# Performance work log

Hardware: AMD Instinct MI355X
Metric: run time of the kernel (lower is better)

## Reference

```python
import jax, jax.numpy as jnp
import numpy as np

H_DIM = 2048
N_HEADS = 16

def setup_inputs() -> dict:
    key = jax.random.key(0)
    ks = jax.random.split(key, 9)
    B, T, C = 2, 2048, H_DIM
    scale = 1.0 / np.sqrt(C)  # lecun_normal approx
    src = jax.random.normal(ks[0], (B, T, C), dtype=jnp.float32)
    Wq = jax.random.normal(ks[1], (C, H_DIM), dtype=jnp.float32) * scale
    Wk = jax.random.normal(ks[2], (C, H_DIM), dtype=jnp.float32) * scale
    Wv = jax.random.normal(ks[3], (C, H_DIM), dtype=jnp.float32) * scale
    Wo = jax.random.normal(ks[4], (H_DIM, H_DIM), dtype=jnp.float32) * scale
    bq = jnp.zeros((H_DIM,), jnp.float32)
    bk = jnp.zeros((H_DIM,), jnp.float32)
    bv = jnp.zeros((H_DIM,), jnp.float32)
    bo = jnp.zeros((H_DIM,), jnp.float32)
    return {"src": src, "Wq": Wq, "bq": bq, "Wk": Wk, "bk": bk,
            "Wv": Wv, "bv": bv, "Wo": Wo, "bo": bo}

def reference(src, Wq, bq, Wk, bk, Wv, bv, Wo, bo):
    B, T, C = src.shape
    N = N_HEADS
    D = C // N
    def heads(x):  # [B,T,h_dim] -> [B,N,T,D]
        return x.reshape(B, T, N, D).transpose(0, 2, 1, 3)
    q = heads(src @ Wq + bq)
    k = heads(src @ Wk + bk)
    v = heads(src @ Wv + bv)
    # scaled dot-product with causal mask
    scores = jnp.einsum('bntd,bnsd->bnts', q, k) / jnp.sqrt(jnp.float32(D))
    causal = jnp.tril(jnp.ones((T, T), dtype=bool))
    scores = jnp.where(causal[None, None], scores, -jnp.inf)
    attn = jax.nn.softmax(scores, axis=-1)
    out = jnp.einsum('bnts,bnsd->bntd', attn, v)  # dropout is identity (drop_p=0)
    out = out.transpose(0, 2, 1, 3).reshape(B, T, N * D)
    return out @ Wo + bo
```

## Files before the change

kernel.cpp:

```cpp
#include <hip/hip_runtime.h>
#include <hip/hip_bf16.h>

typedef float f32x4 __attribute__((ext_vector_type(4)));
typedef __bf16 bf16x8v __attribute__((ext_vector_type(8)));
typedef __bf16 bf16x4v __attribute__((ext_vector_type(4)));
typedef unsigned uint2v __attribute__((ext_vector_type(2)));
typedef bf16x8v __attribute__((may_alias)) bf16x8;
typedef bf16x4v __attribute__((may_alias)) bf16x4;
typedef uint2v __attribute__((may_alias)) u32x2;

typedef __attribute__((address_space(1))) const void gvoid_t;
typedef __attribute__((address_space(3))) void lvoid_t;

#define DEVINL __device__ __forceinline__

#define BDIM 2
#define TDIM 2048
#define CDIM 2048
#define NHEAD 16
#define DHEAD 128
#define MROWS 4096
#define WSZ ((size_t)CDIM * CDIM)
#define XSZ ((size_t)MROWS * CDIM)

#define BARRIER_LGKM() asm volatile("s_waitcnt lgkmcnt(0)\ns_barrier" ::: "memory")

DEVINL __bf16 f2bf(float f) {
  unsigned u = __builtin_bit_cast(unsigned, f);
  u += 0x7fffu + ((u >> 16) & 1u);
  unsigned short h = (unsigned short)(u >> 16);
  return __builtin_bit_cast(__bf16, h);
}

DEVINL unsigned pk2bf_trunc(float lo, float hi) {
  return __builtin_amdgcn_perm(__builtin_bit_cast(unsigned, hi),
                               __builtin_bit_cast(unsigned, lo), 0x07060302);
}

DEVINL void gl2lds16(const void* g, void* l) {
  __builtin_amdgcn_global_load_lds((gvoid_t*)g, (lvoid_t*)l, 16, 0, 0);
}

__global__ void detect_dtype(const unsigned* __restrict__ w,
                             int* __restrict__ flag, int* __restrict__ cnt) {
  const int l = threadIdx.x;
  if (l == 0) *cnt = 0;
  const unsigned word = w[l];
  const unsigned e = (word >> 7) & 0xFFu;
  const int vote = (e >= 0x70u && e <= 0x87u) ? 1 : 0;
  const unsigned long long m = __ballot(vote);
  if (l == 0) *flag = (__popcll(m) >= 32) ? 1 : 0;
}

__global__ __launch_bounds__(256) void cvt_src(const void* __restrict__ in,
                                               __bf16* __restrict__ out,
                                               const int* __restrict__ flag,
                                               int n8) {
  const int i = blockIdx.x * 256 + threadIdx.x;
  if (i >= n8) return;
  if (*flag) {
    ((bf16x8*)out)[i] = ((const bf16x8*)in)[i];
  } else {
    const float* f = (const float*)in + (size_t)i * 8;
    bf16x8v v;
#pragma unroll
    for (int j = 0; j < 8; ++j) v[j] = f2bf(f[j]);
    ((bf16x8*)out)[i] = v;
  }
}

__global__ __launch_bounds__(256) void cvt_wt(
    const void* __restrict__ w0, const void* __restrict__ w1,
    const void* __restrict__ w2, const void* __restrict__ w3,
    __bf16* __restrict__ out, const int* __restrict__ flag) {
  __shared__ __attribute__((aligned(16))) __bf16 tile[64][68];
  const void* W = (blockIdx.z == 0) ? w0 : (blockIdx.z == 1) ? w1
                : (blockIdx.z == 2) ? w2 : w3;
  __bf16* Wt = out + (size_t)blockIdx.z * WSZ;
  const int tx = threadIdx.x & 63, ty = threadIdx.x >> 6;
  const int k0 = blockIdx.x * 64, n0 = blockIdx.y * 64;
  const int fl = *flag;
#pragma unroll
  for (int i = ty; i < 64; i += 4) {
    const size_t off = (size_t)(k0 + i) * CDIM + n0 + tx;
    const float v = fl ? (float)((const __bf16*)W)[off] : ((const float*)W)[off];
    tile[i][tx] = f2bf(v);
  }
  __syncthreads();
#pragma unroll
  for (int i = ty; i < 64; i += 4)
    Wt[(size_t)(n0 + i) * CDIM + k0 + tx] = tile[tx][i];
}

__global__ __launch_bounds__(256) void cvt_bias(
    const void* __restrict__ b0, const void* __restrict__ b1,
    const void* __restrict__ b2, const void* __restrict__ b3,
    float* __restrict__ out, const int* __restrict__ flag) {
  const int i = blockIdx.x * 256 + threadIdx.x;
  const void* b = (i < 2048) ? b0 : (i < 4096) ? b1 : (i < 6144) ? b2 : b3;
  const int idx = i & 2047;
  out[i] = (*flag) ? (float)((const __bf16*)b)[idx] : ((const float*)b)[idx];
}

template <int MODE>
__global__ __launch_bounds__(512, 2) void gemmring(
    const __bf16* __restrict__ A, const __bf16* __restrict__ Bt,
    const float* __restrict__ bias, __bf16* __restrict__ qb,
    __bf16* __restrict__ kb, __bf16* __restrict__ vtb,
    const int* __restrict__ flag, void* __restrict__ outp) {
  constexpr int K = CDIM;
  constexpr int NKT = K / 64;
  __shared__ __attribute__((aligned(16))) __bf16 Asl[4][128 * 32];
  __shared__ __attribute__((aligned(16))) __bf16 Bsl[4][256 * 32];

  const int tid = threadIdx.x;
  const int w = tid >> 6, l = tid & 63;
  const int quad = l >> 4, l16 = l & 15;
  const int wm = w >> 2, wn = w & 3;

  const int bid = blockIdx.x;
  const int bm = bid & 31, bn = bid >> 5;
  const int m0 = bm * 128, n0 = bn * 256;

  const int ls = (tid & 7) ^ ((tid >> 3) & 7);
  const int rbase = 2 * (tid >> 3) + (ls >> 2);
  const int cb8 = (ls & 3) * 8;
  const __bf16* gAh = A + (size_t)(m0 + rbase) * K + cb8;
  const __bf16* gBh = Bt + (size_t)(n0 + rbase) * K + cb8;

  const int L2 = l16 >> 1;
  const int physr = (((l16 & 1) << 2) + quad) ^ L2;
  const int lane_e = L2 * 64 + physr * 8;

#define STAGE_A(h)                                                       \
  gl2lds16(gAh + (size_t)(((h) >> 1) * 64 + ((h) & 1) * 32),             \
           (__bf16*)Asl[(h) & 3] + w * 512)
#define STAGE_B(h, e)                                                    \
  gl2lds16(gBh + (size_t)(e) * 128 * K +                                 \
               (((h) >> 1) * 64 + ((h) & 1) * 32),                       \
           (__bf16*)Bsl[(h) & 3] + (e) * 4096 + w * 512)

  f32x4 acc[4][4];
#pragma unroll
  for (int i = 0; i < 4; ++i)
#pragma unroll
    for (int j = 0; j < 4; ++j) acc[i][j] = (f32x4){0.f, 0.f, 0.f, 0.f};

  STAGE_A(0); STAGE_B(0, 0); STAGE_B(0, 1);
  STAGE_A(1); STAGE_B(1, 0); STAGE_B(1, 1);
  STAGE_A(2); STAGE_B(2, 0); STAGE_B(2, 1);
  asm volatile("s_waitcnt vmcnt(6)" ::: "memory");
  __builtin_amdgcn_sched_barrier(0);
  __builtin_amdgcn_s_barrier();

#define MFMA8(NF0)                                                        \
  __builtin_amdgcn_s_setprio(1);                                          \
  _Pragma("unroll") for (int mi = 0; mi < 4; ++mi) {                      \
    acc[mi][(NF0)] = __builtin_amdgcn_mfma_f32_16x16x32_bf16(             \
        afr[mi], bfr[0], acc[mi][(NF0)], 0, 0, 0);                        \
    acc[mi][(NF0) + 1] = __builtin_amdgcn_mfma_f32_16x16x32_bf16(         \
        afr[mi], bfr[1], acc[mi][(NF0) + 1], 0, 0, 0);                    \
  }                                                                       \
  __builtin_amdgcn_s_setprio(0);

#define LGKM_BAR()                                                        \
  __builtin_amdgcn_s_barrier();                                           \
  asm volatile("s_waitcnt lgkmcnt(0)" ::: "memory");                      \
  __builtin_amdgcn_sched_barrier(0)

  for (int kt = 0; kt < NKT; ++kt) {
    const int h0 = 2 * kt;
    const __bf16* Ab0 = Asl[h0 & 3];
    const __bf16* Bb0 = Bsl[h0 & 3];
    const __bf16* Ab1 = Asl[(h0 + 1) & 3];
    const __bf16* Bb1 = Bsl[(h0 + 1) & 3];
    bf16x8 afr[4], bfr[2];

#pragma unroll
    for (int mi = 0; mi < 4; ++mi)
      afr[mi] = *(const bf16x8*)&Ab0[(wm * 64 + mi * 16) * 32 + lane_e];
    bfr[0] = *(const bf16x8*)&Bb0[(wn * 64 + 0 * 16) * 32 + lane_e];
    bfr[1] = *(const bf16x8*)&Bb0[(wn * 64 + 1 * 16) * 32 + lane_e];
    if (kt <= NKT - 2) { STAGE_A(h0 + 3); STAGE_B(h0 + 3, 0); }
    LGKM_BAR();
    MFMA8(0)
    __builtin_amdgcn_s_barrier();

    bfr[0] = *(const bf16x8*)&Bb0[(wn * 64 + 2 * 16) * 32 + lane_e];
    bfr[1] = *(const bf16x8*)&Bb0[(wn * 64 + 3 * 16) * 32 + lane_e];
    if (kt <= NKT - 2) { STAGE_B(h0 + 3, 1); }
    LGKM_BAR();
    MFMA8(2)
    if (kt < NKT - 1)
      asm volatile("s_waitcnt vmcnt(6)" ::: "memory");
    else
      asm volatile("s_waitcnt vmcnt(0)" ::: "memory");
    __builtin_amdgcn_sched_barrier(0);
    __builtin_amdgcn_s_barrier();

#pragma unroll
    for (int mi = 0; mi < 4; ++mi)
      afr[mi] = *(const bf16x8*)&Ab1[(wm * 64 + mi * 16) * 32 + lane_e];
    bfr[0] = *(const bf16x8*)&Bb1[(wn * 64 + 0 * 16) * 32 + lane_e];
    bfr[1] = *(const bf16x8*)&Bb1[(wn * 64 + 1 * 16) * 32 + lane_e];
    if (kt <= NKT - 3) { STAGE_A(h0 + 4); STAGE_B(h0 + 4, 0); }
    LGKM_BAR();
    MFMA8(0)
    __builtin_amdgcn_s_barrier();

    bfr[0] = *(const bf16x8*)&Bb1[(wn * 64 + 2 * 16) * 32 + lane_e];
    bfr[1] = *(const bf16x8*)&Bb1[(wn * 64 + 3 * 16) * 32 + lane_e];
    if (kt <= NKT - 3) { STAGE_B(h0 + 4, 1); }
    LGKM_BAR();
    MFMA8(2)
    if (kt < NKT - 2)
      asm volatile("s_waitcnt vmcnt(6)" ::: "memory");
    else if (kt == NKT - 2)
      asm volatile("s_waitcnt vmcnt(3)" ::: "memory");
    __builtin_amdgcn_sched_barrier(0);
    __builtin_amdgcn_s_barrier();
  }
#undef MFMA8
#undef LGKM_BAR
#undef STAGE_A
#undef STAGE_B

  if (MODE == 0) {
    const int mat = n0 >> 11;
#pragma unroll
    for (int nf = 0; nf < 4; ++nf) {
      const int n = n0 + wn * 64 + nf * 16 + l16;
      const int nn = n & 2047;
      const int h = nn >> 7, d = nn & 127;
      const float bv = bias[n];
#pragma unroll
      for (int mi = 0; mi < 4; ++mi) {
        const int mbase = m0 + wm * 64 + mi * 16 + quad * 4;
        const int bb = mbase >> 11, t = mbase & 2047;
        if (mat == 2) {
          bf16x4v v4;
#pragma unroll
          for (int r = 0; r < 4; ++r) v4[r] = f2bf(acc[mi][nf][r] + bv);
          *(bf16x4*)&vtb[((size_t)(bb * NHEAD + h) * DHEAD + d) * TDIM + t] = v4;
        } else {
          __bf16* op = (mat == 0) ? qb : kb;
#pragma unroll
          for (int r = 0; r < 4; ++r)
            op[((size_t)(bb * NHEAD + h) * TDIM + t + r) * DHEAD + d] =
                f2bf(acc[mi][nf][r] + bv);
        }
      }
    }
  } else {
    const int ofl = *flag;
#pragma unroll
    for (int nf = 0; nf < 4; ++nf) {
      const int n = n0 + wn * 64 + nf * 16 + l16;
      const float bv = bias[n];
#pragma unroll
      for (int mi = 0; mi < 4; ++mi) {
#pragma unroll
        for (int r = 0; r < 4; ++r) {
          const int m = m0 + wm * 64 + mi * 16 + quad * 4 + r;
          const float v = acc[mi][nf][r] + bv;
          if (ofl) ((__bf16*)outp)[(size_t)m * CDIM + n] = f2bf(v);
          else     ((float*)outp)[(size_t)m * CDIM + n] = v;
        }
      }
    }
  }
}

__global__ __launch_bounds__(256, 2) void attn(
    const __bf16* __restrict__ Q, const __bf16* __restrict__ K,
    const __bf16* __restrict__ Vt, __bf16* __restrict__ ctx,
    int* __restrict__ cnt) {
  constexpr float CSC = 0.12753139726f;
  __shared__ __attribute__((aligned(16))) __bf16 Kls[64 * 128];
  __shared__ __attribute__((aligned(16))) __bf16 Vls[128 * 64];
  __shared__ __attribute__((aligned(16))) __bf16 Pls[4][32 * 64];
  __shared__ int jobLds;

  const int tid = threadIdx.x;
  const int w = tid >> 6, l = tid & 63, quad = l >> 4, l16 = l & 15;

  const int krow = tid >> 4;
  const int kcol = tid & 15;
  const int kldsoff = ((kcol ^ krow) * 8);
  const int vrow = tid >> 3;
  const int vcol = tid & 7;
  const int vldsoff = ((vcol ^ (vrow & 7)) * 8);

  for (;;) {
    __syncthreads();
    if (tid == 0) jobLds = atomicAdd(cnt, 1);
    __syncthreads();
    const int j = jobLds;
    if (j >= 512) break;
    const int qt = 15 - (j >> 5);
    const int bh = j & 31;
    const int t0w = qt * 128 + w * 32;
    const __bf16* Qbh = Q + (size_t)bh * TDIM * DHEAD;
    const __bf16* Kbh = K + (size_t)bh * TDIM * DHEAD;
    const __bf16* Vbh = Vt + (size_t)bh * TDIM * DHEAD;

    bf16x8 qf[2][4];
#pragma unroll
    for (int tt = 0; tt < 2; ++tt)
#pragma unroll
      for (int ks = 0; ks < 4; ++ks)
        qf[tt][ks] = *(const bf16x8*)(Qbh +
                     (size_t)(t0w + tt * 16 + l16) * DHEAD + ks * 32 + quad * 8);

    f32x4 oacc[8][2];
#pragma unroll
    for (int dt = 0; dt < 8; ++dt)
#pragma unroll
      for (int tt = 0; tt < 2; ++tt) oacc[dt][tt] = (f32x4){0.f, 0.f, 0.f, 0.f};
    float mrow[2] = {-1e30f, -1e30f};
    float lrow[2] = {0.f, 0.f};

    const int nsb = 2 * (qt + 1);

    bf16x8 kr[4], vr[4];
#pragma unroll
    for (int p = 0; p < 4; ++p)
      kr[p] = *(const bf16x8*)(Kbh + (size_t)(p * 16 + krow) * DHEAD + kcol * 8);
#pragma unroll
    for (int p = 0; p < 4; ++p)
      vr[p] = *(const bf16x8*)(Vbh + (size_t)(p * 32 + vrow) * TDIM + vcol * 8);

    for (int sb = 0; sb < nsb; ++sb) {
      const int s0 = sb * 64;
      BARRIER_LGKM();
#pragma unroll
      for (int p = 0; p < 4; ++p)
        *(bf16x8*)&Kls[(p * 16 + krow) * 128 + kldsoff] = kr[p];
#pragma unroll
      for (int p = 0; p < 4; ++p)
        *(bf16x8*)&Vls[(p * 32 + vrow) * 64 + vldsoff] = vr[p];
      if (sb + 1 < nsb) {
        const int s1 = s0 + 64;
#pragma unroll
        for (int p = 0; p < 4; ++p)
          kr[p] = *(const bf16x8*)(Kbh + (size_t)(s1 + p * 16 + krow) * DHEAD +
                                   kcol * 8);
#pragma unroll
        for (int p = 0; p < 4; ++p)
          vr[p] = *(const bf16x8*)(Vbh + (size_t)(p * 32 + vrow) * TDIM + s1 +
                                   vcol * 8);
      }
      BARRIER_LGKM();
      if (s0 > t0w + 31) continue;

      f32x4 sacc[4][2];
#pragma unroll
      for (int st = 0; st < 4; ++st)
#pragma unroll
        for (int tt = 0; tt < 2; ++tt) sacc[st][tt] = (f32x4){0.f, 0.f, 0.f, 0.f};
#pragma unroll
      for (int ks = 0; ks < 4; ++ks) {
        bf16x8 kf[4];
#pragma unroll
        for (int st = 0; st < 4; ++st)
          kf[st] = *(const bf16x8*)&Kls[(st * 16 + l16) * 128 +
                                        (((ks * 4 + quad) ^ l16) * 8)];
#pragma unroll
        for (int st = 0; st < 4; ++st)
#pragma unroll
          for (int tt = 0; tt < 2; ++tt)
            sacc[st][tt] = __builtin_amdgcn_mfma_f32_16x16x32_bf16(
                kf[st], qf[tt][ks], sacc[st][tt], 0, 0, 0);
      }
      if (s0 + 63 > t0w) {
#pragma unroll
        for (int st = 0; st < 4; ++st)
#pragma unroll
          for (int tt = 0; tt < 2; ++tt)
#pragma unroll
            for (int r = 0; r < 4; ++r) {
              const int s = s0 + st * 16 + quad * 4 + r;
              const int t = t0w + tt * 16 + l16;
              if (s > t) sacc[st][tt][r] = -1e30f;
            }
      }
#pragma unroll
      for (int tt = 0; tt < 2; ++tt) {
        float vm = -1e30f;
#pragma unroll
        for (int st = 0; st < 4; ++st)
#pragma unroll
          for (int r = 0; r < 4; ++r) vm = fmaxf(vm, sacc[st][tt][r]);
        vm = fmaxf(vm, __shfl_xor(vm, 16));
        vm = fmaxf(vm, __shfl_xor(vm, 32));
        const float mnew = fmaxf(mrow[tt], vm);
        if (__ballot(mnew > mrow[tt])) {
          const float alpha = exp2f((mrow[tt] - mnew) * CSC);
          lrow[tt] *= alpha;
#pragma unroll
          for (int dt = 0; dt < 8; ++dt)
#pragma unroll
            for (int r = 0; r < 4; ++r) oacc[dt][tt][r] *= alpha;
          mrow[tt] = mnew;
        }
        float rs = 0.f;
#pragma unroll
        for (int st = 0; st < 4; ++st) {
          const float p0 = exp2f((sacc[st][tt][0] - mnew) * CSC);
          const float p1 = exp2f((sacc[st][tt][1] - mnew) * CSC);
          const float p2 = exp2f((sacc[st][tt][2] - mnew) * CSC);
          const float p3 = exp2f((sacc[st][tt][3] - mnew) * CSC);
          rs += (p0 + p1) + (p2 + p3);
          u32x2 pk = {pk2bf_trunc(p0, p1), pk2bf_trunc(p2, p3)};
          *(u32x2*)&Pls[w][(tt * 16 + l16) * 64 +
                           (((st * 2 + (quad >> 1)) ^ (l16 & 7)) * 8) +
                           (quad & 1) * 4] = pk;
        }
        rs += __shfl_xor(rs, 16);
        rs += __shfl_xor(rs, 32);
        lrow[tt] += rs;
      }
      asm volatile("s_waitcnt lgkmcnt(0)" ::: "memory");
#pragma unroll
      for (int ks = 0; ks < 2; ++ks) {
        bf16x8 pf[2];
#pragma unroll
        for (int tt = 0; tt < 2; ++tt)
          pf[tt] = *(const bf16x8*)&Pls[w][(tt * 16 + l16) * 64 +
                                           (((ks * 4 + quad) ^ (l16 & 7)) * 8)];
#pragma unroll
        for (int dt = 0; dt < 8; ++dt) {
          const bf16x8 vf =
              *(const bf16x8*)&Vls[(dt * 16 + l16) * 64 +
                                   (((ks * 4 + quad) ^ (l16 & 7)) * 8)];
#pragma unroll
          for (int tt = 0; tt < 2; ++tt)
            oacc[dt][tt] = __builtin_amdgcn_mfma_f32_16x16x32_bf16(
                vf, pf[tt], oacc[dt][tt], 0, 0, 0);
        }
      }
    }

    const int b = bh >> 4, h = bh & 15;
#pragma unroll
    for (int tt = 0; tt < 2; ++tt) {
      const float rinv = 1.0f / lrow[tt];
      const int t = t0w + tt * 16 + l16;
      __bf16* cp = ctx + ((size_t)(b * TDIM + t)) * CDIM + h * DHEAD;
#pragma unroll
      for (int dt = 0; dt < 8; ++dt) {
        bf16x4v v4;
#pragma unroll
        for (int r = 0; r < 4; ++r) v4[r] = f2bf(oacc[dt][tt][r] * rinv);
        *(bf16x4*)&cp[dt * 16 + quad * 4] = v4;
      }
    }
  }
}

extern "C" void kernel_launch(void* const* d_in, const int* in_sizes, int n_in,
                              void* d_out, int out_size, void* d_ws,
                              size_t ws_size, hipStream_t stream) {
  const void* src = d_in[0];
  const void* Wq = d_in[1];
  const void* bq = d_in[2];
  const void* Wk = d_in[3];
  const void* bk = d_in[4];
  const void* Wv = d_in[5];
  const void* bv = d_in[6];
  const void* Wo = d_in[7];
  const void* bo = d_in[8];

  char* wsb = (char*)d_ws;
  int* flag = (int*)wsb;
  int* cnt = (int*)(wsb + 128);
  __bf16* srcbf = (__bf16*)(wsb + 256);
  __bf16* wqt = srcbf + XSZ;
  __bf16* wkt = wqt + WSZ;
  __bf16* wvt = wkt + WSZ;
  __bf16* wot = wvt + WSZ;
  __bf16* qb = wot + WSZ;
  __bf16* kb = qb + XSZ;
  __bf16* vtb = kb + XSZ;
  float* biasf = (float*)(vtb + XSZ);
  __bf16* ctx = srcbf;

  detect_dtype<<<1, 64, 0, stream>>>((const unsigned*)src, flag, cnt);
  cvt_src<<<4096, 256, 0, stream>>>(src, srcbf, flag, (int)(XSZ / 8));
  cvt_wt<<<dim3(32, 32, 4), 256, 0, stream>>>(Wq, Wk, Wv, Wo, wqt, flag);
  cvt_bias<<<32, 256, 0, stream>>>(bq, bk, bv, bo, biasf, flag);
  gemmring<0><<<768, 512, 0, stream>>>(srcbf, wqt, biasf, qb, kb, vtb,
                                       nullptr, nullptr);
  attn<<<512, 256, 0, stream>>>(qb, kb, vtb, ctx, cnt);
  gemmring<1><<<256, 512, 0, stream>>>(ctx, wot, biasf + 6144, nullptr,
                                       nullptr, nullptr, flag, d_out);
}
```

Measured before the change: 426.6 us.

## Inline dtype detection, fuse bias conversion, lazy softmax rescale, MFMA priority

Removes the separate dtype-detect and bias-conversion launches by running a per-wave detection inside each kernel and folding bias conversion into extra blocks of the source-conversion kernel, with a memset for the counter. In attention, the running-max rescale is skipped unless the new max exceeds the old by a threshold, which cuts rescale work but lets exponentials run against a stale max. s_setprio is raised around the MFMA loops to favour matrix issue. Each wave now re-reads the source words to detect dtype, which adds small redundant loads.

```diff
diff --git a/kernel.cpp b/kernel.cpp
--- a/kernel.cpp
+++ b/kernel.cpp
@@ -41,24 +41,32 @@
   __builtin_amdgcn_global_load_lds((gvoid_t*)g, (lvoid_t*)l, 16, 0, 0);
 }
 
-__global__ void detect_dtype(const unsigned* __restrict__ w,
-                             int* __restrict__ flag, int* __restrict__ cnt) {
-  const int l = threadIdx.x;
-  if (l == 0) *cnt = 0;
+DEVINL int wave_detect(const unsigned* __restrict__ w) {
+  const int l = threadIdx.x & 63;
   const unsigned word = w[l];
   const unsigned e = (word >> 7) & 0xFFu;
   const int vote = (e >= 0x70u && e <= 0x87u) ? 1 : 0;
   const unsigned long long m = __ballot(vote);
-  if (l == 0) *flag = (__popcll(m) >= 32) ? 1 : 0;
-}
-
-__global__ __launch_bounds__(256) void cvt_src(const void* __restrict__ in,
-                                               __bf16* __restrict__ out,
-                                               const int* __restrict__ flag,
-                                               int n8) {
-  const int i = blockIdx.x * 256 + threadIdx.x;
+  return (__popcll(m) >= 32) ? 1 : 0;
+}
+
+__global__ __launch_bounds__(256) void cvt_src(
+    const void* __restrict__ in, __bf16* __restrict__ out, int n8,
+    const void* __restrict__ b0, const void* __restrict__ b1,
+    const void* __restrict__ b2, const void* __restrict__ b3,
+    float* __restrict__ biasf) {
+  const int fl = wave_detect((const unsigned*)in);
+  const int bi = blockIdx.x;
+  if (bi >= 4096) {
+    const int i = (bi - 4096) * 256 + threadIdx.x;
+    const void* b = (i < 2048) ? b0 : (i < 4096) ? b1 : (i < 6144) ? b2 : b3;
+    const int idx = i & 2047;
+    biasf[i] = fl ? (float)((const __bf16*)b)[idx] : ((const float*)b)[idx];
+    return;
+  }
+  const int i = bi * 256 + threadIdx.x;
   if (i >= n8) return;
-  if (*flag) {
+  if (fl) {
     ((bf16x8*)out)[i] = ((const bf16x8*)in)[i];
   } else {
     const float* f = (const float*)in + (size_t)i * 8;
@@ -72,14 +80,14 @@
 __global__ __launch_bounds__(256) void cvt_wt(
     const void* __restrict__ w0, const void* __restrict__ w1,
     const void* __restrict__ w2, const void* __restrict__ w3,
-    __bf16* __restrict__ out, const int* __restrict__ flag) {
+    __bf16* __restrict__ out, const unsigned* __restrict__ srcw) {
   __shared__ __attribute__((aligned(16))) __bf16 tile[64][68];
   const void* W = (blockIdx.z == 0) ? w0 : (blockIdx.z == 1) ? w1
                 : (blockIdx.z == 2) ? w2 : w3;
   __bf16* Wt = out + (size_t)blockIdx.z * WSZ;
   const int tx = threadIdx.x & 63, ty = threadIdx.x >> 6;
   const int k0 = blockIdx.x * 64, n0 = blockIdx.y * 64;
-  const int fl = *flag;
+  const int fl = wave_detect(srcw);
 #pragma unroll
   for (int i = ty; i < 64; i += 4) {
     const size_t off = (size_t)(k0 + i) * CDIM + n0 + tx;
@@ -92,22 +100,12 @@
     Wt[(size_t)(n0 + i) * CDIM + k0 + tx] = tile[tx][i];
 }
 
-__global__ __launch_bounds__(256) void cvt_bias(
-    const void* __restrict__ b0, const void* __restrict__ b1,
-    const void* __restrict__ b2, const void* __restrict__ b3,
-    float* __restrict__ out, const int* __restrict__ flag) {
-  const int i = blockIdx.x * 256 + threadIdx.x;
-  const void* b = (i < 2048) ? b0 : (i < 4096) ? b1 : (i < 6144) ? b2 : b3;
-  const int idx = i & 2047;
-  out[i] = (*flag) ? (float)((const __bf16*)b)[idx] : ((const float*)b)[idx];
-}
-
 template <int MODE>
 __global__ __launch_bounds__(512, 2) void gemmring(
     const __bf16* __restrict__ A, const __bf16* __restrict__ Bt,
     const float* __restrict__ bias, __bf16* __restrict__ qb,
     __bf16* __restrict__ kb, __bf16* __restrict__ vtb,
-    const int* __restrict__ flag, void* __restrict__ outp) {
+    const unsigned* __restrict__ srcw, void* __restrict__ outp) {
   constexpr int K = CDIM;
   constexpr int NKT = K / 64;
   __shared__ __attribute__((aligned(16))) __bf16 Asl[4][128 * 32];
@@ -252,7 +250,7 @@
       }
     }
   } else {
-    const int ofl = *flag;
+    const int ofl = wave_detect(srcw);
 #pragma unroll
     for (int nf = 0; nf < 4; ++nf) {
       const int n = n0 + wn * 64 + nf * 16 + l16;
@@ -358,6 +356,7 @@
       for (int st = 0; st < 4; ++st)
 #pragma unroll
         for (int tt = 0; tt < 2; ++tt) sacc[st][tt] = (f32x4){0.f, 0.f, 0.f, 0.f};
+      __builtin_amdgcn_s_setprio(1);
 #pragma unroll
       for (int ks = 0; ks < 4; ++ks) {
         bf16x8 kf[4];
@@ -372,6 +371,7 @@
             sacc[st][tt] = __builtin_amdgcn_mfma_f32_16x16x32_bf16(
                 kf[st], qf[tt][ks], sacc[st][tt], 0, 0, 0);
       }
+      __builtin_amdgcn_s_setprio(0);
       if (s0 + 63 > t0w) {
 #pragma unroll
         for (int st = 0; st < 4; ++st)
@@ -393,23 +393,24 @@
           for (int r = 0; r < 4; ++r) vm = fmaxf(vm, sacc[st][tt][r]);
         vm = fmaxf(vm, __shfl_xor(vm, 16));
         vm = fmaxf(vm, __shfl_xor(vm, 32));
-        const float mnew = fmaxf(mrow[tt], vm);
-        if (__ballot(mnew > mrow[tt])) {
-          const float alpha = exp2f((mrow[tt] - mnew) * CSC);
+        if (__ballot((vm - mrow[tt]) * CSC > 8.0f)) {
+          const float mn = fmaxf(mrow[tt], vm);
+          const float alpha = exp2f((mrow[tt] - mn) * CSC);
           lrow[tt] *= alpha;
 #pragma unroll
           for (int dt = 0; dt < 8; ++dt)
 #pragma unroll
             for (int r = 0; r < 4; ++r) oacc[dt][tt][r] *= alpha;
-          mrow[tt] = mnew;
+          mrow[tt] = mn;
         }
+        const float mcur = mrow[tt];
         float rs = 0.f;
 #pragma unroll
         for (int st = 0; st < 4; ++st) {
-          const float p0 = exp2f((sacc[st][tt][0] - mnew) * CSC);
-          const float p1 = exp2f((sacc[st][tt][1] - mnew) * CSC);
-          const float p2 = exp2f((sacc[st][tt][2] - mnew) * CSC);
-          const float p3 = exp2f((sacc[st][tt][3] - mnew) * CSC);
+          const float p0 = exp2f((sacc[st][tt][0] - mcur) * CSC);
+          const float p1 = exp2f((sacc[st][tt][1] - mcur) * CSC);
+          const float p2 = exp2f((sacc[st][tt][2] - mcur) * CSC);
+          const float p3 = exp2f((sacc[st][tt][3] - mcur) * CSC);
           rs += (p0 + p1) + (p2 + p3);
           u32x2 pk = {pk2bf_trunc(p0, p1), pk2bf_trunc(p2, p3)};
           *(u32x2*)&Pls[w][(tt * 16 + l16) * 64 +
@@ -421,6 +422,7 @@
         lrow[tt] += rs;
       }
       asm volatile("s_waitcnt lgkmcnt(0)" ::: "memory");
+      __builtin_amdgcn_s_setprio(1);
 #pragma unroll
       for (int ks = 0; ks < 2; ++ks) {
         bf16x8 pf[2];
@@ -439,6 +441,7 @@
                 vf, pf[tt], oacc[dt][tt], 0, 0, 0);
         }
       }
+      __builtin_amdgcn_s_setprio(0);
     }
 
     const int b = bh >> 4, h = bh & 15;
@@ -472,7 +475,6 @@
   const void* bo = d_in[8];
 
   char* wsb = (char*)d_ws;
-  int* flag = (int*)wsb;
   int* cnt = (int*)(wsb + 128);
   __bf16* srcbf = (__bf16*)(wsb + 256);
   __bf16* wqt = srcbf + XSZ;
@@ -484,14 +486,17 @@
   __bf16* vtb = kb + XSZ;
   float* biasf = (float*)(vtb + XSZ);
   __bf16* ctx = srcbf;
-
-  detect_dtype<<<1, 64, 0, stream>>>((const unsigned*)src, flag, cnt);
-  cvt_src<<<4096, 256, 0, stream>>>(src, srcbf, flag, (int)(XSZ / 8));
-  cvt_wt<<<dim3(32, 32, 4), 256, 0, stream>>>(Wq, Wk, Wv, Wo, wqt, flag);
-  cvt_bias<<<32, 256, 0, stream>>>(bq, bk, bv, bo, biasf, flag);
+  (void)wkt; (void)wvt;
+
+  hipMemsetAsync(cnt, 0, sizeof(int), stream);
+  cvt_src<<<4128, 256, 0, stream>>>(src, srcbf, (int)(XSZ / 8), bq, bk, bv,
+                                    bo, biasf);
+  cvt_wt<<<dim3(32, 32, 4), 256, 0, stream>>>(Wq, Wk, Wv, Wo, wqt,
+                                              (const unsigned*)src);
   gemmring<0><<<768, 512, 0, stream>>>(srcbf, wqt, biasf, qb, kb, vtb,
                                        nullptr, nullptr);
   attn<<<512, 256, 0, stream>>>(qb, kb, vtb, ctx, cnt);
   gemmring<1><<<256, 512, 0, stream>>>(ctx, wot, biasf + 6144, nullptr,
-                                       nullptr, nullptr, flag, d_out);
-}
+                                       nullptr, nullptr, (const unsigned*)src,
+                                       d_out);
+}
```

Result: faster. 415.1 us (-2.7%).
